# Optimization experiments

Measured on AMD Instinct MI355X. Metric: run time of the kernel, lower is better.

The kernel has to match this reference:

```python
import jax, jax.numpy as jnp
from jax import lax
import numpy as np

NUM_INPUTS = 512
NUM_HIDDENS = 1024
BATCH = 64
SEQ_LEN = 512


def setup_inputs() -> dict:
    key = jax.random.key(0)
    ks = jax.random.split(key, 8)
    D, H = NUM_INPUTS, NUM_HIDDENS
    w = lambda k, shape: 0.01 * jax.random.normal(k, shape, dtype=jnp.float32)
    return {
        "inputs": jax.random.normal(ks[0], (BATCH, SEQ_LEN, D), dtype=jnp.float32),
        "state": jax.random.normal(ks[1], (BATCH, H), dtype=jnp.float32),
        "W_xz": w(ks[2], (D, H)), "W_hz": w(ks[3], (H, H)), "b_z": jnp.zeros((H,), jnp.float32),
        "W_xr": w(ks[4], (D, H)), "W_hr": w(ks[5], (H, H)), "b_r": jnp.zeros((H,), jnp.float32),
        "W_xh": w(ks[6], (D, H)), "W_hh": w(ks[7], (H, H)), "b_h": jnp.zeros((H,), jnp.float32),
    }


def reference(inputs, state, W_xz, W_hz, b_z, W_xr, W_hr, b_r, W_xh, W_hh, b_h):
    B, T, _ = inputs.shape
    Hd = state.shape[1]
    # Precompute all input-side gate projections in three big GEMMs: [T, B, H]
    xz = (jnp.einsum('btd,dh->bth', inputs, W_xz) + b_z).transpose(1, 0, 2)
    xr = (jnp.einsum('btd,dh->bth', inputs, W_xr) + b_r).transpose(1, 0, 2)
    xh = (jnp.einsum('btd,dh->bth', inputs, W_xh) + b_h).transpose(1, 0, 2)

    def step(Hc, xs):
        xz_t, xr_t, xh_t = xs
        Z = jax.nn.sigmoid(xz_t + Hc @ W_hz)
        R = jax.nn.sigmoid(xr_t + Hc @ W_hr)
        H_tilda = jnp.tanh(xh_t + (R * Hc) @ W_hh)
        Hn = Z * Hc + (1.0 - Z) * H_tilda
        return Hn, Hn

    H_final, outs = lax.scan(step, state, (xz, xr, xh))  # outs: [T, B, H]
    # torch.cat(outputs, 0) -> [T*B, H]; .transpose(1, 0) -> [H, T*B]
    outputs = outs.reshape(T * B, Hd).T
    return outputs, H_final
```

## Files before the change

### kernel.cpp

```cpp
#include <hip/hip_runtime.h>
#include <hip/hip_bf16.h>

typedef unsigned short ushort_t;
typedef unsigned int uint32;
typedef unsigned long long ull;
typedef short bf16x8 __attribute__((ext_vector_type(8)));
typedef float f32x4 __attribute__((ext_vector_type(4)));

#define Bb 64
#define Tt 512
#define Dd 512
#define Hh 1024
#define KK 1536
#define NBLK 64
#define OUT2_OFF 33554432ull
#define FLAGS_OFF 9699328ull
#define XB_OFF    9707776ull
#define XB_BYTES  33554432ull


__device__ inline ushort_t f2b(float f) {
    __hip_bfloat16 h = __float2bfloat16(f);
    return __builtin_bit_cast(ushort_t, h);
}
__device__ inline float b2f(ushort_t u) {
    uint32 x = ((uint32)u) << 16;
    return __builtin_bit_cast(float, x);
}
__device__ inline bf16x8 ld_bf8(const ushort_t* p) {
    uint4 v = *reinterpret_cast<const uint4*>(p);
    return __builtin_bit_cast(bf16x8, v);
}
__device__ inline bf16x8 ld_x8(const float* p) {
    float4 u = *reinterpret_cast<const float4*>(p);
    float4 v = *reinterpret_cast<const float4*>(p + 4);
    bf16x8 a;
    a[0] = (short)f2b(u.x); a[1] = (short)f2b(u.y); a[2] = (short)f2b(u.z); a[3] = (short)f2b(u.w);
    a[4] = (short)f2b(v.x); a[5] = (short)f2b(v.y); a[6] = (short)f2b(v.z); a[7] = (short)f2b(v.w);
    return a;
}
__device__ inline uint4 ld_c16(const ushort_t* p) {
    uint4 d;
    asm volatile("global_load_dwordx4 %0, %1, off sc0 sc1" : "=v"(d) : "v"(p) : "memory");
    return d;
}
__device__ inline bf16x8 as_bf(uint4 v) { return __builtin_bit_cast(bf16x8, v); }
__device__ inline void st_a8(ushort_t* p, ull v) {
    __hip_atomic_store((ull*)p, v, __ATOMIC_RELAXED, __HIP_MEMORY_SCOPE_AGENT);
}
__device__ inline uint32 ld_flag(const uint32* p) {
    return __hip_atomic_load(p, __ATOMIC_RELAXED, __HIP_MEMORY_SCOPE_AGENT);
}
__device__ inline float sigm(float x) { return 1.f / (1.f + __expf(-x)); }

#define MFMA(a, b, c) __builtin_amdgcn_mfma_f32_16x16x32_bf16((a), (b), (c), 0, 0, 0)

__global__ __launch_bounds__(256) void k_init(const float* __restrict__ state,
                                              ushort_t* __restrict__ HB, uint32* flags) {
    int i = blockIdx.x * 256 + threadIdx.x;
    if (i < Bb * Hh) HB[i] = f2b(state[i]);
    if (i < 2112) flags[i] = 0;
}

__global__ __launch_bounds__(256) void k_xb(const float* __restrict__ inp,
                                            ushort_t* __restrict__ XB) {
    size_t i = ((size_t)blockIdx.x * 256 + threadIdx.x) * 8;
    bf16x8 v = ld_x8(inp + i);
    *reinterpret_cast<uint4*>(XB + i) = __builtin_bit_cast(uint4, v);
}

__global__ __launch_bounds__(256) void k_wt(const float* __restrict__ Wxz, const float* __restrict__ Whz,
                                            const float* __restrict__ Wxr, const float* __restrict__ Whr,
                                            const float* __restrict__ Wxh, const float* __restrict__ Whh,
                                            ushort_t* __restrict__ WT) {
    __shared__ float lds[64][65];
    int id = blockIdx.x;
    int g = id / 384, rem = id % 384, nt = rem / 24, kt = rem % 24;
    const float* Wx = (g == 0) ? Wxz : (g == 1) ? Wxr : Wxh;
    const float* Wh = (g == 0) ? Whz : (g == 1) ? Whr : Whh;
    int n0 = nt * 64, k0 = kt * 64;
    int tr = threadIdx.x >> 6, tc = threadIdx.x & 63;
    #pragma unroll
    for (int i = 0; i < 16; i++) {
        int kl = i * 4 + tr, k = k0 + kl;
        lds[kl][tc] = (k < 512) ? Wx[(size_t)k * Hh + n0 + tc]
                                : Wh[(size_t)(k - 512) * Hh + n0 + tc];
    }
    __syncthreads();
    #pragma unroll
    for (int i = 0; i < 16; i++) {
        int nl = i * 4 + tr;
        WT[((size_t)g * Hh + n0 + nl) * KK + k0 + tc] = f2b(lds[tc][nl]);
    }
}

__global__ __launch_bounds__(256, 1) void gru_persist(
    const float* __restrict__ inp, const ushort_t* __restrict__ XB, int use_xb,
    const float* __restrict__ bz, const float* __restrict__ br, const float* __restrict__ bh,
    ushort_t* HB, ushort_t* RH, const ushort_t* __restrict__ WT,
    uint32* flags, float* __restrict__ out) {
    __shared__ ushort_t WL[3 * 48 * 512];
    __shared__ ushort_t STG[4 * 256];

    const int bi = blockIdx.x;
    const int tid = threadIdx.x;

    for (int idx = tid; idx < 9216; idx += 256) {
        int g = idx / 3072, r = idx % 3072, col = r / 192, c8 = r % 192;
        int kc = c8 >> 2, slot = c8 & 3, ps = slot ^ ((col >> 1) & 3);
        const ushort_t* src = WT + ((size_t)g * Hh + bi * 16 + col) * KK + c8 * 8;
        *reinterpret_cast<uint4*>(WL + g * 24576 + kc * 512 + col * 32 + ps * 8) =
            *reinterpret_cast<const uint4*>(src);
    }

    const int l = tid & 63, w = tid >> 6;
    const int lrow = l & 15, lq = l >> 4;
    const int ncol = bi * 16 + lrow;
    const int wloff = lrow * 32 + (lq ^ ((lrow >> 1) & 3)) * 8;
    const int c0 = (bi + w) & 3;

    #define WTILE(g, kc) ld_bf8(WL + (g) * 24576 + (kc) * 512 + wloff)

    const int arow = w * 16 + lrow;
    const float*    xF = inp + (size_t)arow * (Tt * Dd) + lq * 8;
    const ushort_t* xBp = XB + (size_t)arow * (Tt * Dd) + lq * 8;
    const ushort_t* hb = HB + arow * Hh + lq * 8;
    const ushort_t* rb = RH + arow * Hh + lq * 8;
    const float bzv = bz[ncol], brv = br[ncol], bhv = bh[ncol];

    const size_t strow  = (size_t)(w * 16 + (l >> 2)) * Hh + bi * 16 + (l & 3) * 4;
    const int    stg_wr = w * 256;
    const int    stg_rd = w * 256 + (l >> 2) * 16 + (l & 3) * 4;

    float hold[4];
    #pragma unroll
    for (int j = 0; j < 4; j++)
        hold[j] = b2f(HB[(size_t)(w * 16 + lq * 4 + j) * Hh + ncol]);

    __syncthreads();

    const f32x4 z4 = {0.f, 0.f, 0.f, 0.f};
    f32x4 az = z4, ar = z4, ahx = z4;

    bf16x8 xa[16];
    if (use_xb) {
        #pragma unroll
        for (int i = 0; i < 16; i++) xa[i] = ld_bf8(xBp + i * 32);
    } else {
        #pragma unroll
        for (int i = 0; i < 16; i++) xa[i] = ld_x8(xF + i * 32);
    }
    #pragma unroll
    for (int kk = 0; kk < 16; kk++) {
        az  = MFMA(xa[kk], WTILE(0, kk), az);
        ar  = MFMA(xa[kk], WTILE(1, kk), ar);
        ahx = MFMA(xa[kk], WTILE(2, kk), ahx);
    }

    for (int t = 0; t < Tt; ++t) {
        const uint32 valH = 2u * (uint32)t;
        const uint32 valR = 2u * (uint32)t + 1u;

        {
            uint32 v = ld_flag(flags + l * 32);
            if (__all((int)(v >= valH))) {
                uint4 A[32];
                #pragma unroll
                for (int i = 0; i < 32; i++) A[i] = ld_c16(hb + i * 32);
                asm volatile("s_waitcnt vmcnt(0)" ::: "memory");
                __builtin_amdgcn_sched_barrier(0);
                #pragma unroll
                for (int kk = 0; kk < 32; kk++) {
                    az = MFMA(as_bf(A[kk]), WTILE(0, 16 + kk), az);
                    ar = MFMA(as_bf(A[kk]), WTILE(1, 16 + kk), ar);
                }
            } else {
                for (int ci = 0; ci < 4; ci++) {
                    int c = (c0 + ci) & 3;
                    uint32 vv = ld_flag(flags + (c * 16 + (l & 15)) * 32);
                    while (__any((int)(vv < valH))) {
                        __builtin_amdgcn_s_sleep(1);
                        vv = ld_flag(flags + (c * 16 + (l & 15)) * 32);
                    }
                    uint4 A[8];
                    #pragma unroll
                    for (int i = 0; i < 8; i++) A[i] = ld_c16(hb + (c * 8 + i) * 32);
                    asm volatile("s_waitcnt vmcnt(0)" ::: "memory");
                    __builtin_amdgcn_sched_barrier(0);
                    #pragma unroll
                    for (int i = 0; i < 8; i++) {
                        int kk = c * 8 + i;
                        az = MFMA(as_bf(A[i]), WTILE(0, 16 + kk), az);
                        ar = MFMA(as_bf(A[i]), WTILE(1, 16 + kk), ar);
                    }
                }
            }
        }
        float zreg[4];
        #pragma unroll
        for (int j = 0; j < 4; j++) {
            zreg[j] = sigm(az[j] + bzv);
            float rr = sigm(ar[j] + brv);
            STG[stg_wr + (lq * 4 + j) * 16 + lrow] = f2b(rr * hold[j]);
        }
        asm volatile("s_waitcnt lgkmcnt(0)" ::: "memory");
        st_a8(RH + strow, *reinterpret_cast<const ull*>(&STG[stg_rd]));
        asm volatile("s_waitcnt vmcnt(0)" ::: "memory");
        __syncthreads();
        if (tid == 0)
            __hip_atomic_store(flags + (uint32)bi * 32, valR,
                               __ATOMIC_RELAXED, __HIP_MEMORY_SCOPE_AGENT);

        if (t < Tt - 1) {
            if (use_xb) {
                #pragma unroll
                for (int i = 0; i < 16; i++) xa[i] = ld_bf8(xBp + (size_t)(t + 1) * Dd + i * 32);
            } else {
                #pragma unroll
                for (int i = 0; i < 16; i++) xa[i] = ld_x8(xF + (size_t)(t + 1) * Dd + i * 32);
            }
        }

        f32x4 ah0 = ahx, ah1 = z4;
        {
            uint32 v = ld_flag(flags + l * 32);
            if (__all((int)(v >= valR))) {
                uint4 A[32];
                #pragma unroll
                for (int i = 0; i < 32; i++) A[i] = ld_c16(rb + i * 32);
                asm volatile("s_waitcnt vmcnt(0)" ::: "memory");
                __builtin_amdgcn_sched_barrier(0);
                #pragma unroll
                for (int kk = 0; kk < 32; kk += 2) {
                    ah0 = MFMA(as_bf(A[kk]),     WTILE(2, 16 + kk),     ah0);
                    ah1 = MFMA(as_bf(A[kk + 1]), WTILE(2, 16 + kk + 1), ah1);
                }
            } else {
                for (int ci = 0; ci < 4; ci++) {
                    int c = (c0 + ci) & 3;
                    uint32 vv = ld_flag(flags + (c * 16 + (l & 15)) * 32);
                    while (__any((int)(vv < valR))) {
                        __builtin_amdgcn_s_sleep(1);
                        vv = ld_flag(flags + (c * 16 + (l & 15)) * 32);
                    }
                    uint4 A[8];
                    #pragma unroll
                    for (int i = 0; i < 8; i++) A[i] = ld_c16(rb + (c * 8 + i) * 32);
                    asm volatile("s_waitcnt vmcnt(0)" ::: "memory");
                    __builtin_amdgcn_sched_barrier(0);
                    #pragma unroll
                    for (int i = 0; i < 8; i++) {
                        int kk = c * 8 + i;
                        if (i & 1) ah1 = MFMA(as_bf(A[i]), WTILE(2, 16 + kk), ah1);
                        else       ah0 = MFMA(as_bf(A[i]), WTILE(2, 16 + kk), ah0);
                    }
                }
            }
        }
        f32x4 aht = ah0 + ah1;
        float hn[4];
        #pragma unroll
        for (int j = 0; j < 4; j++) {
            float pre = aht[j] + bhv;
            float e = __expf(-2.f * fabsf(pre));
            float th = (1.f - e) / (1.f + e);
            th = copysignf(th, pre);
            float v = zreg[j] * hold[j] + (1.f - zreg[j]) * th;
            hold[j] = v;
            hn[j] = v;
            STG[stg_wr + (lq * 4 + j) * 16 + lrow] = f2b(v);
        }
        asm volatile("s_waitcnt lgkmcnt(0)" ::: "memory");
        st_a8(HB + strow, *reinterpret_cast<const ull*>(&STG[stg_rd]));
        asm volatile("s_waitcnt vmcnt(0)" ::: "memory");
        __syncthreads();
        if (tid == 0)
            __hip_atomic_store(flags + (uint32)bi * 32, valR + 1u,
                               __ATOMIC_RELAXED, __HIP_MEMORY_SCOPE_AGENT);

        *reinterpret_cast<float4*>(out + (size_t)ncol * (Tt * Bb) + (size_t)t * Bb + w * 16 + lq * 4) =
            make_float4(hn[0], hn[1], hn[2], hn[3]);
        if (t == Tt - 1) {
            #pragma unroll
            for (int j = 0; j < 4; j++)
                out[OUT2_OFF + (size_t)(w * 16 + lq * 4 + j) * Hh + ncol] = hn[j];
        }

        az = z4; ar = z4; ahx = z4;
        if (t < Tt - 1) {
            #pragma unroll
            for (int kk = 0; kk < 16; kk++) {
                az  = MFMA(xa[kk], WTILE(0, kk), az);
                ar  = MFMA(xa[kk], WTILE(1, kk), ar);
                ahx = MFMA(xa[kk], WTILE(2, kk), ahx);
            }
        }
    }
    #undef WTILE
}

extern "C" void kernel_launch(void* const* d_in, const int* in_sizes, int n_in,
                              void* d_out, int out_size, void* d_ws, size_t ws_size,
                              hipStream_t stream) {
    const float* inp   = (const float*)d_in[0];
    const float* state = (const float*)d_in[1];
    const float* Wxz   = (const float*)d_in[2];
    const float* Whz   = (const float*)d_in[3];
    const float* bz    = (const float*)d_in[4];
    const float* Wxr   = (const float*)d_in[5];
    const float* Whr   = (const float*)d_in[6];
    const float* br    = (const float*)d_in[7];
    const float* Wxh   = (const float*)d_in[8];
    const float* Whh   = (const float*)d_in[9];
    const float* bh    = (const float*)d_in[10];
    float* out = (float*)d_out;

    char* ws = (char*)d_ws;
    ushort_t* HB    = (ushort_t*)(ws);
    ushort_t* RH    = (ushort_t*)(ws + 131072);
    ushort_t* WT    = (ushort_t*)(ws + 262144);
    uint32*   flags = (uint32*)(ws + FLAGS_OFF);
    ushort_t* XB    = (ushort_t*)(ws + XB_OFF);
    int use_xb = (ws_size >= XB_OFF + XB_BYTES) ? 1 : 0;

    k_init<<<dim3(256), dim3(256), 0, stream>>>(state, HB, flags);
    k_wt<<<dim3(1152), dim3(256), 0, stream>>>(Wxz, Whz, Wxr, Whr, Wxh, Whh, WT);
    if (use_xb)
        k_xb<<<dim3(8192), dim3(256), 0, stream>>>(inp, XB);

    void* args[] = {(void*)&inp, (void*)&XB, (void*)&use_xb,
                    (void*)&bz, (void*)&br, (void*)&bh,
                    (void*)&HB, (void*)&RH, (void*)&WT, (void*)&flags, (void*)&out};
    hipError_t e = hipLaunchCooperativeKernel((const void*)gru_persist, dim3(NBLK), dim3(256),
                                              args, 0, stream);
    if (e != hipSuccess) {
        gru_persist<<<dim3(NBLK), dim3(256), 0, stream>>>(inp, XB, use_xb, bz, br, bh,
                                                          HB, RH, WT, flags, out);
    }
}
```

Measured before the change: 8.664 ms.

## Split GRU persistent kernel into 32 blocks with split-K reduction across waves

```diff
diff --git a/kernel.cpp b/kernel.cpp
--- a/kernel.cpp
+++ b/kernel.cpp
@@ -12,10 +12,10 @@
 #define Dd 512
 #define Hh 1024
 #define KK 1536
-#define NBLK 64
+#define NBLK 32
 #define OUT2_OFF 33554432ull
 #define FLAGS_OFF 9699328ull
-#define XB_OFF    9707776ull
+#define XB_OFF    9728000ull
 #define XB_BYTES  33554432ull
 
 
@@ -94,114 +94,159 @@
     }
 }
 
-__global__ __launch_bounds__(256, 1) void gru_persist(
+__global__ __launch_bounds__(512, 2) void gru_persist(
     const float* __restrict__ inp, const ushort_t* __restrict__ XB, int use_xb,
     const float* __restrict__ bz, const float* __restrict__ br, const float* __restrict__ bh,
     ushort_t* HB, ushort_t* RH, const ushort_t* __restrict__ WT,
     uint32* flags, float* __restrict__ out) {
-    __shared__ ushort_t WL[3 * 48 * 512];
-    __shared__ ushort_t STG[4 * 256];
+    __shared__ ushort_t WX[2 * 2 * 16 * 512];
+    __shared__ float    RED[8 * 8 * 64 * 4];
+    __shared__ ushort_t STG[8 * 256];
 
     const int bi = blockIdx.x;
     const int tid = threadIdx.x;
-
-    for (int idx = tid; idx < 9216; idx += 256) {
-        int g = idx / 3072, r = idx % 3072, col = r / 192, c8 = r % 192;
-        int kc = c8 >> 2, slot = c8 & 3, ps = slot ^ ((col >> 1) & 3);
-        const ushort_t* src = WT + ((size_t)g * Hh + bi * 16 + col) * KK + c8 * 8;
-        *reinterpret_cast<uint4*>(WL + g * 24576 + kc * 512 + col * 32 + ps * 8) =
-            *reinterpret_cast<const uint4*>(src);
-    }
-
     const int l = tid & 63, w = tid >> 6;
     const int lrow = l & 15, lq = l >> 4;
-    const int ncol = bi * 16 + lrow;
     const int wloff = lrow * 32 + (lq ^ ((lrow >> 1) & 3)) * 8;
-    const int c0 = (bi + w) & 3;
-
-    #define WTILE(g, kc) ld_bf8(WL + (g) * 24576 + (kc) * 512 + wloff)
-
-    const int arow = w * 16 + lrow;
-    const float*    xF = inp + (size_t)arow * (Tt * Dd) + lq * 8;
-    const ushort_t* xBp = XB + (size_t)arow * (Tt * Dd) + lq * 8;
-    const ushort_t* hb = HB + arow * Hh + lq * 8;
-    const ushort_t* rb = RH + arow * Hh + lq * 8;
+
+    for (int idx = tid; idx < 4096; idx += 512) {
+        int tile = idx >> 6, chunk = idx & 63;
+        int g = tile >> 5, nt = (tile >> 4) & 1, ks = tile & 15;
+        int col = chunk >> 2, slot = chunk & 3;
+        const ushort_t* src = WT + ((size_t)g * Hh + bi * 32 + nt * 16 + col) * KK + ks * 32 + slot * 8;
+        *reinterpret_cast<uint4*>(WX + ((g * 2 + nt) * 16 + ks) * 512 + col * 32 +
+                                  (slot ^ ((col >> 1) & 3)) * 8) =
+            *reinterpret_cast<const uint4*>(src);
+    }
+    #define WXT(g, nt, ks) ld_bf8(WX + (((g) * 2 + (nt)) * 16 + (ks)) * 512 + wloff)
+
+    bf16x8 Wzh[2][4], Wrh[2][4], Whh_[2][4], Whx[2][2];
+    #pragma unroll
+    for (int nt = 0; nt < 2; nt++) {
+        #pragma unroll
+        for (int j = 0; j < 4; j++) {
+            const ushort_t* base = WT + ((size_t)0 * Hh + bi * 32 + nt * 16 + lrow) * KK
+                                      + 512 + w * 128 + j * 32 + lq * 8;
+            Wzh[nt][j]  = ld_bf8(base);
+            Wrh[nt][j]  = ld_bf8(base + (size_t)Hh * KK);
+            Whh_[nt][j] = ld_bf8(base + (size_t)2 * Hh * KK);
+        }
+        #pragma unroll
+        for (int j = 0; j < 2; j++)
+            Whx[nt][j] = ld_bf8(WT + ((size_t)2 * Hh + bi * 32 + nt * 16 + lrow) * KK
+                                   + w * 64 + j * 32 + lq * 8);
+    }
+
+    const ushort_t* hbB = HB + (size_t)lrow * Hh + w * 128 + lq * 8;
+    const ushort_t* rbB = RH + (size_t)lrow * Hh + w * 128 + lq * 8;
+    const float*    xFb = inp + (size_t)lrow * (Tt * Dd) + w * 64 + lq * 8;
+    const ushort_t* xBb = XB + (size_t)lrow * (Tt * Dd) + w * 64 + lq * 8;
+
+    const int fm = w >> 1, fn = w & 1;
+    const int ncol = bi * 32 + fn * 16 + lrow;
     const float bzv = bz[ncol], brv = br[ncol], bhv = bh[ncol];
-
-    const size_t strow  = (size_t)(w * 16 + (l >> 2)) * Hh + bi * 16 + (l & 3) * 4;
-    const int    stg_wr = w * 256;
-    const int    stg_rd = w * 256 + (l >> 2) * 16 + (l & 3) * 4;
+    const size_t strow = (size_t)(fm * 16 + (l >> 2)) * Hh + bi * 32 + fn * 16 + (l & 3) * 4;
+    ushort_t* stW = &STG[w * 256];
+    const int stg_rd = w * 256 + (l >> 2) * 16 + (l & 3) * 4;
 
     float hold[4];
     #pragma unroll
     for (int j = 0; j < 4; j++)
-        hold[j] = b2f(HB[(size_t)(w * 16 + lq * 4 + j) * Hh + ncol]);
+        hold[j] = b2f(HB[(size_t)(fm * 16 + lq * 4 + j) * Hh + ncol]);
 
     __syncthreads();
 
     const f32x4 z4 = {0.f, 0.f, 0.f, 0.f};
-    f32x4 az = z4, ar = z4, ahx = z4;
-
-    bf16x8 xa[16];
-    if (use_xb) {
-        #pragma unroll
-        for (int i = 0; i < 16; i++) xa[i] = ld_bf8(xBp + i * 32);
-    } else {
-        #pragma unroll
-        for (int i = 0; i < 16; i++) xa[i] = ld_x8(xF + i * 32);
-    }
-    #pragma unroll
-    for (int kk = 0; kk < 16; kk++) {
-        az  = MFMA(xa[kk], WTILE(0, kk), az);
-        ar  = MFMA(xa[kk], WTILE(1, kk), ar);
-        ahx = MFMA(xa[kk], WTILE(2, kk), ahx);
-    }
+    #define RED_AT(tile, src) reinterpret_cast<f32x4*>(&RED[(((tile) * 8 + (src)) * 64 + l) * 4])
 
     for (int t = 0; t < Tt; ++t) {
         const uint32 valH = 2u * (uint32)t;
         const uint32 valR = 2u * (uint32)t + 1u;
 
         {
-            uint32 v = ld_flag(flags + l * 32);
-            if (__all((int)(v >= valH))) {
-                uint4 A[32];
-                #pragma unroll
-                for (int i = 0; i < 32; i++) A[i] = ld_c16(hb + i * 32);
-                asm volatile("s_waitcnt vmcnt(0)" ::: "memory");
-                __builtin_amdgcn_sched_barrier(0);
-                #pragma unroll
-                for (int kk = 0; kk < 32; kk++) {
-                    az = MFMA(as_bf(A[kk]), WTILE(0, 16 + kk), az);
-                    ar = MFMA(as_bf(A[kk]), WTILE(1, 16 + kk), ar);
-                }
-            } else {
-                for (int ci = 0; ci < 4; ci++) {
-                    int c = (c0 + ci) & 3;
-                    uint32 vv = ld_flag(flags + (c * 16 + (l & 15)) * 32);
-                    while (__any((int)(vv < valH))) {
-                        __builtin_amdgcn_s_sleep(1);
-                        vv = ld_flag(flags + (c * 16 + (l & 15)) * 32);
-                    }
-                    uint4 A[8];
-                    #pragma unroll
-                    for (int i = 0; i < 8; i++) A[i] = ld_c16(hb + (c * 8 + i) * 32);
-                    asm volatile("s_waitcnt vmcnt(0)" ::: "memory");
-                    __builtin_amdgcn_sched_barrier(0);
-                    #pragma unroll
-                    for (int i = 0; i < 8; i++) {
-                        int kk = c * 8 + i;
-                        az = MFMA(as_bf(A[i]), WTILE(0, 16 + kk), az);
-                        ar = MFMA(as_bf(A[i]), WTILE(1, 16 + kk), ar);
-                    }
+            uint32 v = ld_flag(flags + (l & 31) * 32);
+            if (!__all((int)(v >= valH))) {
+                uint32 vv = ld_flag(flags + (w * 4 + (l & 3)) * 32);
+                while (__any((int)(vv < valH))) {
+                    __builtin_amdgcn_s_sleep(1);
+                    vv = ld_flag(flags + (w * 4 + (l & 3)) * 32);
                 }
             }
         }
+        uint4 Hf[16];
+        #pragma unroll
+        for (int m = 0; m < 4; m++)
+            #pragma unroll
+            for (int j = 0; j < 4; j++)
+                Hf[m * 4 + j] = ld_c16(hbB + (size_t)m * 16 * Hh + j * 32);
+        asm volatile("s_waitcnt vmcnt(0)" ::: "memory");
+        __builtin_amdgcn_sched_barrier(0);
+
+        bf16x8 xf[8];
+        if (use_xb) {
+            #pragma unroll
+            for (int m = 0; m < 4; m++)
+                #pragma unroll
+                for (int j = 0; j < 2; j++)
+                    xf[m * 2 + j] = ld_bf8(xBb + (size_t)m * 16 * (Tt * Dd) + (size_t)t * Dd + j * 32);
+        } else {
+            #pragma unroll
+            for (int m = 0; m < 4; m++)
+                #pragma unroll
+                for (int j = 0; j < 2; j++)
+                    xf[m * 2 + j] = ld_x8(xFb + (size_t)m * 16 * (Tt * Dd) + (size_t)t * Dd + j * 32);
+        }
+
+        {
+            f32x4 acc[8];
+            #pragma unroll
+            for (int m = 0; m < 4; m++)
+                #pragma unroll
+                for (int nt = 0; nt < 2; nt++) {
+                    f32x4 a = z4;
+                    #pragma unroll
+                    for (int j = 0; j < 4; j++) a = MFMA(as_bf(Hf[m * 4 + j]), Wzh[nt][j], a);
+                    #pragma unroll
+                    for (int j = 0; j < 2; j++) a = MFMA(xf[m * 2 + j], WXT(0, nt, w * 2 + j), a);
+                    acc[m * 2 + nt] = a;
+                }
+            #pragma unroll
+            for (int i = 0; i < 8; i++) *RED_AT(i, w) = acc[i];
+        }
+        __syncthreads();
+        f32x4 azf = z4;
+        #pragma unroll
+        for (int s = 0; s < 8; s++) azf += *RED_AT(w, s);
+        __syncthreads();
+
+        {
+            f32x4 acc[8];
+            #pragma unroll
+            for (int m = 0; m < 4; m++)
+                #pragma unroll
+                for (int nt = 0; nt < 2; nt++) {
+                    f32x4 a = z4;
+                    #pragma unroll
+                    for (int j = 0; j < 4; j++) a = MFMA(as_bf(Hf[m * 4 + j]), Wrh[nt][j], a);
+                    #pragma unroll
+                    for (int j = 0; j < 2; j++) a = MFMA(xf[m * 2 + j], WXT(1, nt, w * 2 + j), a);
+                    acc[m * 2 + nt] = a;
+                }
+            #pragma unroll
+            for (int i = 0; i < 8; i++) *RED_AT(i, w) = acc[i];
+        }
+        __syncthreads();
+        f32x4 arf = z4;
+        #pragma unroll
+        for (int s = 0; s < 8; s++) arf += *RED_AT(w, s);
+        __syncthreads();
+
         float zreg[4];
         #pragma unroll
         for (int j = 0; j < 4; j++) {
-            zreg[j] = sigm(az[j] + bzv);
-            float rr = sigm(ar[j] + brv);
-            STG[stg_wr + (lq * 4 + j) * 16 + lrow] = f2b(rr * hold[j]);
+            zreg[j] = sigm(azf[j] + bzv);
+            float rr = sigm(arf[j] + brv);
+            stW[(lq * 4 + j) * 16 + lrow] = f2b(rr * hold[j]);
         }
         asm volatile("s_waitcnt lgkmcnt(0)" ::: "memory");
         st_a8(RH + strow, *reinterpret_cast<const ull*>(&STG[stg_rd]));
@@ -211,64 +256,58 @@
             __hip_atomic_store(flags + (uint32)bi * 32, valR,
                                __ATOMIC_RELAXED, __HIP_MEMORY_SCOPE_AGENT);
 
-        if (t < Tt - 1) {
-            if (use_xb) {
-                #pragma unroll
-                for (int i = 0; i < 16; i++) xa[i] = ld_bf8(xBp + (size_t)(t + 1) * Dd + i * 32);
-            } else {
-                #pragma unroll
-                for (int i = 0; i < 16; i++) xa[i] = ld_x8(xF + (size_t)(t + 1) * Dd + i * 32);
+        {
+            uint32 v = ld_flag(flags + (l & 31) * 32);
+            if (!__all((int)(v >= valR))) {
+                uint32 vv = ld_flag(flags + (w * 4 + (l & 3)) * 32);
+                while (__any((int)(vv < valR))) {
+                    __builtin_amdgcn_s_sleep(1);
+                    vv = ld_flag(flags + (w * 4 + (l & 3)) * 32);
+                }
             }
         }
-
-        f32x4 ah0 = ahx, ah1 = z4;
-        {
-            uint32 v = ld_flag(flags + l * 32);
-            if (__all((int)(v >= valR))) {
-                uint4 A[32];
-                #pragma unroll
-                for (int i = 0; i < 32; i++) A[i] = ld_c16(rb + i * 32);
-                asm volatile("s_waitcnt vmcnt(0)" ::: "memory");
-                __builtin_amdgcn_sched_barrier(0);
-                #pragma unroll
-                for (int kk = 0; kk < 32; kk += 2) {
-                    ah0 = MFMA(as_bf(A[kk]),     WTILE(2, 16 + kk),     ah0);
-                    ah1 = MFMA(as_bf(A[kk + 1]), WTILE(2, 16 + kk + 1), ah1);
-                }
-            } else {
-                for (int ci = 0; ci < 4; ci++) {
-                    int c = (c0 + ci) & 3;
-                    uint32 vv = ld_flag(flags + (c * 16 + (l & 15)) * 32);
-                    while (__any((int)(vv < valR))) {
-                        __builtin_amdgcn_s_sleep(1);
-                        vv = ld_flag(flags + (c * 16 + (l & 15)) * 32);
-                    }
-                    uint4 A[8];
-                    #pragma unroll
-                    for (int i = 0; i < 8; i++) A[i] = ld_c16(rb + (c * 8 + i) * 32);
-                    asm volatile("s_waitcnt vmcnt(0)" ::: "memory");
-                    __builtin_amdgcn_sched_barrier(0);
-                    #pragma unroll
-                    for (int i = 0; i < 8; i++) {
-                        int kk = c * 8 + i;
-                        if (i & 1) ah1 = MFMA(as_bf(A[i]), WTILE(2, 16 + kk), ah1);
-                        else       ah0 = MFMA(as_bf(A[i]), WTILE(2, 16 + kk), ah0);
-                    }
-                }
-            }
-        }
-        f32x4 aht = ah0 + ah1;
+        uint4 Rf[16];
+        #pragma unroll
+        for (int m = 0; m < 4; m++)
+            #pragma unroll
+            for (int j = 0; j < 4; j++)
+                Rf[m * 4 + j] = ld_c16(rbB + (size_t)m * 16 * Hh + j * 32);
+        asm volatile("s_waitcnt vmcnt(0)" ::: "memory");
+        __builtin_amdgcn_sched_barrier(0);
+
+        {
+            f32x4 acc[8];
+            #pragma unroll
+            for (int m = 0; m < 4; m++)
+                #pragma unroll
+                for (int nt = 0; nt < 2; nt++) {
+                    f32x4 a = z4;
+                    #pragma unroll
+                    for (int j = 0; j < 4; j++) a = MFMA(as_bf(Rf[m * 4 + j]), Whh_[nt][j], a);
+                    #pragma unroll
+                    for (int j = 0; j < 2; j++) a = MFMA(xf[m * 2 + j], Whx[nt][j], a);
+                    acc[m * 2 + nt] = a;
+                }
+            #pragma unroll
+            for (int i = 0; i < 8; i++) *RED_AT(i, w) = acc[i];
+        }
+        __syncthreads();
+        f32x4 ahf = z4;
+        #pragma unroll
+        for (int s = 0; s < 8; s++) ahf += *RED_AT(w, s);
+        __syncthreads();
+
         float hn[4];
         #pragma unroll
         for (int j = 0; j < 4; j++) {
-            float pre = aht[j] + bhv;
+            float pre = ahf[j] + bhv;
             float e = __expf(-2.f * fabsf(pre));
             float th = (1.f - e) / (1.f + e);
             th = copysignf(th, pre);
             float v = zreg[j] * hold[j] + (1.f - zreg[j]) * th;
             hold[j] = v;
             hn[j] = v;
-            STG[stg_wr + (lq * 4 + j) * 16 + lrow] = f2b(v);
+            stW[(lq * 4 + j) * 16 + lrow] = f2b(v);
         }
         asm volatile("s_waitcnt lgkmcnt(0)" ::: "memory");
         st_a8(HB + strow, *reinterpret_cast<const ull*>(&STG[stg_rd]));
@@ -278,25 +317,16 @@
             __hip_atomic_store(flags + (uint32)bi * 32, valR + 1u,
                                __ATOMIC_RELAXED, __HIP_MEMORY_SCOPE_AGENT);
 
-        *reinterpret_cast<float4*>(out + (size_t)ncol * (Tt * Bb) + (size_t)t * Bb + w * 16 + lq * 4) =
+        *reinterpret_cast<float4*>(out + (size_t)ncol * (Tt * Bb) + (size_t)t * Bb + fm * 16 + lq * 4) =
             make_float4(hn[0], hn[1], hn[2], hn[3]);
         if (t == Tt - 1) {
             #pragma unroll
             for (int j = 0; j < 4; j++)
-                out[OUT2_OFF + (size_t)(w * 16 + lq * 4 + j) * Hh + ncol] = hn[j];
-        }
-
-        az = z4; ar = z4; ahx = z4;
-        if (t < Tt - 1) {
-            #pragma unroll
-            for (int kk = 0; kk < 16; kk++) {
-                az  = MFMA(xa[kk], WTILE(0, kk), az);
-                ar  = MFMA(xa[kk], WTILE(1, kk), ar);
-                ahx = MFMA(xa[kk], WTILE(2, kk), ahx);
-            }
-        }
-    }
-    #undef WTILE
+                out[OUT2_OFF + (size_t)(fm * 16 + lq * 4 + j) * Hh + ncol] = hn[j];
+        }
+    }
+    #undef WXT
+    #undef RED_AT
 }
 
 extern "C" void kernel_launch(void* const* d_in, const int* in_sizes, int n_in,
@@ -331,10 +361,10 @@
     void* args[] = {(void*)&inp, (void*)&XB, (void*)&use_xb,
                     (void*)&bz, (void*)&br, (void*)&bh,
                     (void*)&HB, (void*)&RH, (void*)&WT, (void*)&flags, (void*)&out};
-    hipError_t e = hipLaunchCooperativeKernel((const void*)gru_persist, dim3(NBLK), dim3(256),
+    hipError_t e = hipLaunchCooperativeKernel((const void*)gru_persist, dim3(NBLK), dim3(512),
                                               args, 0, stream);
     if (e != hipSuccess) {
-        gru_persist<<<dim3(NBLK), dim3(256), 0, stream>>>(inp, XB, use_xb, bz, br, bh,
+        gru_persist<<<dim3(NBLK), dim3(512), 0, stream>>>(inp, XB, use_xb, bz, br, bh,
                                                           HB, RH, WT, flags, out);
     }
 }
```

Result: slower. 11.05 ms (+27.6%).

## Use per-timestep ring buffers for hidden and reset states to allow cached loads

Applied to the files above, without the earlier changes.

```diff
diff --git a/kernel.cpp b/kernel.cpp
--- a/kernel.cpp
+++ b/kernel.cpp
@@ -14,10 +14,17 @@
 #define KK 1536
 #define NBLK 64
 #define OUT2_OFF 33554432ull
-#define FLAGS_OFF 9699328ull
-#define XB_OFF    9707776ull
-#define XB_BYTES  33554432ull
-
+
+#define WT_OFF      262144ull
+#define FLAGS_OFF   9699328ull
+#define XB_SMALL    9728000ull
+#define HBR_OFF     16777216ull
+#define RING_BYTES  67633152ull
+#define RHR_OFF     (HBR_OFF + RING_BYTES)
+#define XB_BIG      (RHR_OFF + RING_BYTES)
+#define NEED_RING   XB_BIG
+#define NEED_XB_BIG (XB_BIG + 33554432ull)
+#define NEED_XB_SM  (XB_SMALL + 33554432ull)
 
 __device__ inline ushort_t f2b(float f) {
     __hip_bfloat16 h = __float2bfloat16(f);
@@ -56,9 +63,9 @@
 #define MFMA(a, b, c) __builtin_amdgcn_mfma_f32_16x16x32_bf16((a), (b), (c), 0, 0, 0)
 
 __global__ __launch_bounds__(256) void k_init(const float* __restrict__ state,
-                                              ushort_t* __restrict__ HB, uint32* flags) {
+                                              ushort_t* __restrict__ HB0, uint32* flags) {
     int i = blockIdx.x * 256 + threadIdx.x;
-    if (i < Bb * Hh) HB[i] = f2b(state[i]);
+    if (i < Bb * Hh) HB0[i] = f2b(state[i]);
     if (i < 2112) flags[i] = 0;
 }
 
@@ -94,10 +101,11 @@
     }
 }
 
+template <int RING>
 __global__ __launch_bounds__(256, 1) void gru_persist(
     const float* __restrict__ inp, const ushort_t* __restrict__ XB, int use_xb,
     const float* __restrict__ bz, const float* __restrict__ br, const float* __restrict__ bh,
-    ushort_t* HB, ushort_t* RH, const ushort_t* __restrict__ WT,
+    ushort_t* HBR, ushort_t* RHR, const ushort_t* __restrict__ WT,
     uint32* flags, float* __restrict__ out) {
     __shared__ ushort_t WL[3 * 48 * 512];
     __shared__ ushort_t STG[4 * 256];
@@ -124,8 +132,8 @@
     const int arow = w * 16 + lrow;
     const float*    xF = inp + (size_t)arow * (Tt * Dd) + lq * 8;
     const ushort_t* xBp = XB + (size_t)arow * (Tt * Dd) + lq * 8;
-    const ushort_t* hb = HB + arow * Hh + lq * 8;
-    const ushort_t* rb = RH + arow * Hh + lq * 8;
+    const ushort_t* hb = HBR + arow * Hh + lq * 8;
+    const ushort_t* rb = RHR + arow * Hh + lq * 8;
     const float bzv = bz[ncol], brv = br[ncol], bhv = bh[ncol];
 
     const size_t strow  = (size_t)(w * 16 + (l >> 2)) * Hh + bi * 16 + (l & 3) * 4;
@@ -135,7 +143,7 @@
     float hold[4];
     #pragma unroll
     for (int j = 0; j < 4; j++)
-        hold[j] = b2f(HB[(size_t)(w * 16 + lq * 4 + j) * Hh + ncol]);
+        hold[j] = b2f(HBR[(size_t)(w * 16 + lq * 4 + j) * Hh + ncol]);
 
     __syncthreads();
 
@@ -160,19 +168,31 @@
     for (int t = 0; t < Tt; ++t) {
         const uint32 valH = 2u * (uint32)t;
         const uint32 valR = 2u * (uint32)t + 1u;
+        const size_t tb  = RING ? ((size_t)t << 16) : 0;
+        const size_t tb1 = RING ? ((size_t)(t + 1) << 16) : 0;
 
         {
             uint32 v = ld_flag(flags + l * 32);
             if (__all((int)(v >= valH))) {
-                uint4 A[32];
-                #pragma unroll
-                for (int i = 0; i < 32; i++) A[i] = ld_c16(hb + i * 32);
-                asm volatile("s_waitcnt vmcnt(0)" ::: "memory");
-                __builtin_amdgcn_sched_barrier(0);
-                #pragma unroll
-                for (int kk = 0; kk < 32; kk++) {
-                    az = MFMA(as_bf(A[kk]), WTILE(0, 16 + kk), az);
-                    ar = MFMA(as_bf(A[kk]), WTILE(1, 16 + kk), ar);
+                asm volatile("" ::: "memory");
+                if (RING) {
+                    #pragma unroll
+                    for (int kk = 0; kk < 32; kk++) {
+                        bf16x8 A = ld_bf8(hb + tb + kk * 32);
+                        az = MFMA(A, WTILE(0, 16 + kk), az);
+                        ar = MFMA(A, WTILE(1, 16 + kk), ar);
+                    }
+                } else {
+                    uint4 A[32];
+                    #pragma unroll
+                    for (int i = 0; i < 32; i++) A[i] = ld_c16(hb + i * 32);
+                    asm volatile("s_waitcnt vmcnt(0)" ::: "memory");
+                    __builtin_amdgcn_sched_barrier(0);
+                    #pragma unroll
+                    for (int kk = 0; kk < 32; kk++) {
+                        az = MFMA(as_bf(A[kk]), WTILE(0, 16 + kk), az);
+                        ar = MFMA(as_bf(A[kk]), WTILE(1, 16 + kk), ar);
+                    }
                 }
             } else {
                 for (int ci = 0; ci < 4; ci++) {
@@ -182,16 +202,27 @@
                         __builtin_amdgcn_s_sleep(1);
                         vv = ld_flag(flags + (c * 16 + (l & 15)) * 32);
                     }
-                    uint4 A[8];
-                    #pragma unroll
-                    for (int i = 0; i < 8; i++) A[i] = ld_c16(hb + (c * 8 + i) * 32);
-                    asm volatile("s_waitcnt vmcnt(0)" ::: "memory");
-                    __builtin_amdgcn_sched_barrier(0);
-                    #pragma unroll
-                    for (int i = 0; i < 8; i++) {
-                        int kk = c * 8 + i;
-                        az = MFMA(as_bf(A[i]), WTILE(0, 16 + kk), az);
-                        ar = MFMA(as_bf(A[i]), WTILE(1, 16 + kk), ar);
+                    asm volatile("" ::: "memory");
+                    if (RING) {
+                        #pragma unroll
+                        for (int i = 0; i < 8; i++) {
+                            int kk = c * 8 + i;
+                            bf16x8 A = ld_bf8(hb + tb + kk * 32);
+                            az = MFMA(A, WTILE(0, 16 + kk), az);
+                            ar = MFMA(A, WTILE(1, 16 + kk), ar);
+                        }
+                    } else {
+                        uint4 A[8];
+                        #pragma unroll
+                        for (int i = 0; i < 8; i++) A[i] = ld_c16(hb + (c * 8 + i) * 32);
+                        asm volatile("s_waitcnt vmcnt(0)" ::: "memory");
+                        __builtin_amdgcn_sched_barrier(0);
+                        #pragma unroll
+                        for (int i = 0; i < 8; i++) {
+                            int kk = c * 8 + i;
+                            az = MFMA(as_bf(A[i]), WTILE(0, 16 + kk), az);
+                            ar = MFMA(as_bf(A[i]), WTILE(1, 16 + kk), ar);
+                        }
                     }
                 }
             }
@@ -204,7 +235,7 @@
             STG[stg_wr + (lq * 4 + j) * 16 + lrow] = f2b(rr * hold[j]);
         }
         asm volatile("s_waitcnt lgkmcnt(0)" ::: "memory");
-        st_a8(RH + strow, *reinterpret_cast<const ull*>(&STG[stg_rd]));
+        st_a8(RHR + strow + tb, *reinterpret_cast<const ull*>(&STG[stg_rd]));
         asm volatile("s_waitcnt vmcnt(0)" ::: "memory");
         __syncthreads();
         if (tid == 0)
@@ -225,15 +256,26 @@
         {
             uint32 v = ld_flag(flags + l * 32);
             if (__all((int)(v >= valR))) {
-                uint4 A[32];
-                #pragma unroll
-                for (int i = 0; i < 32; i++) A[i] = ld_c16(rb + i * 32);
-                asm volatile("s_waitcnt vmcnt(0)" ::: "memory");
-                __builtin_amdgcn_sched_barrier(0);
-                #pragma unroll
-                for (int kk = 0; kk < 32; kk += 2) {
-                    ah0 = MFMA(as_bf(A[kk]),     WTILE(2, 16 + kk),     ah0);
-                    ah1 = MFMA(as_bf(A[kk + 1]), WTILE(2, 16 + kk + 1), ah1);
+                asm volatile("" ::: "memory");
+                if (RING) {
+                    #pragma unroll
+                    for (int kk = 0; kk < 32; kk += 2) {
+                        bf16x8 A0 = ld_bf8(rb + tb + kk * 32);
+                        bf16x8 A1 = ld_bf8(rb + tb + kk * 32 + 32);
+                        ah0 = MFMA(A0, WTILE(2, 16 + kk),     ah0);
+                        ah1 = MFMA(A1, WTILE(2, 16 + kk + 1), ah1);
+                    }
+                } else {
+                    uint4 A[32];
+                    #pragma unroll
+                    for (int i = 0; i < 32; i++) A[i] = ld_c16(rb + i * 32);
+                    asm volatile("s_waitcnt vmcnt(0)" ::: "memory");
+                    __builtin_amdgcn_sched_barrier(0);
+                    #pragma unroll
+                    for (int kk = 0; kk < 32; kk += 2) {
+                        ah0 = MFMA(as_bf(A[kk]),     WTILE(2, 16 + kk),     ah0);
+                        ah1 = MFMA(as_bf(A[kk + 1]), WTILE(2, 16 + kk + 1), ah1);
+                    }
                 }
             } else {
                 for (int ci = 0; ci < 4; ci++) {
@@ -243,16 +285,27 @@
                         __builtin_amdgcn_s_sleep(1);
                         vv = ld_flag(flags + (c * 16 + (l & 15)) * 32);
                     }
-                    uint4 A[8];
-                    #pragma unroll
-                    for (int i = 0; i < 8; i++) A[i] = ld_c16(rb + (c * 8 + i) * 32);
-                    asm volatile("s_waitcnt vmcnt(0)" ::: "memory");
-                    __builtin_amdgcn_sched_barrier(0);
-                    #pragma unroll
-                    for (int i = 0; i < 8; i++) {
-                        int kk = c * 8 + i;
-                        if (i & 1) ah1 = MFMA(as_bf(A[i]), WTILE(2, 16 + kk), ah1);
-                        else       ah0 = MFMA(as_bf(A[i]), WTILE(2, 16 + kk), ah0);
+                    asm volatile("" ::: "memory");
+                    if (RING) {
+                        #pragma unroll
+                        for (int i = 0; i < 8; i++) {
+                            int kk = c * 8 + i;
+                            bf16x8 A = ld_bf8(rb + tb + kk * 32);
+                            if (i & 1) ah1 = MFMA(A, WTILE(2, 16 + kk), ah1);
+                            else       ah0 = MFMA(A, WTILE(2, 16 + kk), ah0);
+                        }
+                    } else {
+                        uint4 A[8];
+                        #pragma unroll
+                        for (int i = 0; i < 8; i++) A[i] = ld_c16(rb + (c * 8 + i) * 32);
+                        asm volatile("s_waitcnt vmcnt(0)" ::: "memory");
+                        __builtin_amdgcn_sched_barrier(0);
+                        #pragma unroll
+                        for (int i = 0; i < 8; i++) {
+                            int kk = c * 8 + i;
+                            if (i & 1) ah1 = MFMA(as_bf(A[i]), WTILE(2, 16 + kk), ah1);
+                            else       ah0 = MFMA(as_bf(A[i]), WTILE(2, 16 + kk), ah0);
+                        }
                     }
                 }
             }
@@ -271,7 +324,7 @@
             STG[stg_wr + (lq * 4 + j) * 16 + lrow] = f2b(v);
         }
         asm volatile("s_waitcnt lgkmcnt(0)" ::: "memory");
-        st_a8(HB + strow, *reinterpret_cast<const ull*>(&STG[stg_rd]));
+        st_a8(HBR + strow + tb1, *reinterpret_cast<const ull*>(&STG[stg_rd]));
         asm volatile("s_waitcnt vmcnt(0)" ::: "memory");
         __syncthreads();
         if (tid == 0)
@@ -316,12 +369,15 @@
     float* out = (float*)d_out;
 
     char* ws = (char*)d_ws;
-    ushort_t* HB    = (ushort_t*)(ws);
-    ushort_t* RH    = (ushort_t*)(ws + 131072);
-    ushort_t* WT    = (ushort_t*)(ws + 262144);
+    ushort_t* WT    = (ushort_t*)(ws + WT_OFF);
     uint32*   flags = (uint32*)(ws + FLAGS_OFF);
-    ushort_t* XB    = (ushort_t*)(ws + XB_OFF);
-    int use_xb = (ws_size >= XB_OFF + XB_BYTES) ? 1 : 0;
+
+    const int ring = (ws_size >= NEED_RING) ? 1 : 0;
+    ushort_t* HB = ring ? (ushort_t*)(ws + HBR_OFF) : (ushort_t*)ws;
+    ushort_t* RH = ring ? (ushort_t*)(ws + RHR_OFF) : (ushort_t*)(ws + 131072);
+    ushort_t* XB = ring ? (ushort_t*)(ws + XB_BIG)  : (ushort_t*)(ws + XB_SMALL);
+    int use_xb = ring ? (ws_size >= NEED_XB_BIG ? 1 : 0)
+                      : (ws_size >= NEED_XB_SM  ? 1 : 0);
 
     k_init<<<dim3(256), dim3(256), 0, stream>>>(state, HB, flags);
     k_wt<<<dim3(1152), dim3(256), 0, stream>>>(Wxz, Whz, Wxr, Whr, Wxh, Whh, WT);
@@ -331,10 +387,14 @@
     void* args[] = {(void*)&inp, (void*)&XB, (void*)&use_xb,
                     (void*)&bz, (void*)&br, (void*)&bh,
                     (void*)&HB, (void*)&RH, (void*)&WT, (void*)&flags, (void*)&out};
-    hipError_t e = hipLaunchCooperativeKernel((const void*)gru_persist, dim3(NBLK), dim3(256),
-                                              args, 0, stream);
+    const void* fn = ring ? (const void*)gru_persist<1> : (const void*)gru_persist<0>;
+    hipError_t e = hipLaunchCooperativeKernel(fn, dim3(NBLK), dim3(256), args, 0, stream);
     if (e != hipSuccess) {
-        gru_persist<<<dim3(NBLK), dim3(256), 0, stream>>>(inp, XB, use_xb, bz, br, bh,
-                                                          HB, RH, WT, flags, out);
-    }
-}
+        if (ring)
+            gru_persist<1><<<dim3(NBLK), dim3(256), 0, stream>>>(inp, XB, use_xb, bz, br, bh,
+                                                                 HB, RH, WT, flags, out);
+        else
+            gru_persist<0><<<dim3(NBLK), dim3(256), 0, stream>>>(inp, XB, use_xb, bz, br, bh,
+                                                                 HB, RH, WT, flags, out);
+    }
+}
```

Result: slower. 9.130 ms (+5.4%).
